# Kernel optimization log

Measured on AMD Instinct MI355X. Metric: run time of the kernel, lower is better.

The kernel has to match this reference:

```python
import jax, jax.numpy as jnp
import numpy as np

B, T, I, H = 64, 2048, 256, 256


def setup_inputs() -> dict:
    key = jax.random.key(0)
    ks = jax.random.split(key, 6)
    s = 1.0 / np.sqrt(H)
    x = jax.random.normal(ks[0], (B, T, I), dtype=jnp.float32)
    att_weights = jax.random.uniform(ks[1], (B, T), dtype=jnp.float32)
    lengths = jax.random.randint(ks[2], (B,), 1, T + 1, dtype=jnp.int32)
    W_ih = jax.random.uniform(ks[3], (3 * H, I), minval=-s, maxval=s, dtype=jnp.float32)
    W_hh = jax.random.uniform(ks[4], (3 * H, H), minval=-s, maxval=s, dtype=jnp.float32)
    b_ih = jax.random.uniform(ks[5], (3 * H,), minval=-s, maxval=s, dtype=jnp.float32)
    b_hh = jax.random.uniform(jax.random.fold_in(key, 7), (3 * H,), minval=-s, maxval=s, dtype=jnp.float32)
    return {"x": x, "att_weights": att_weights, "lengths": lengths,
            "W_ih": W_ih, "W_hh": W_hh, "b_ih": b_ih, "b_hh": b_hh}


def reference(x, att_weights, lengths, W_ih, W_hh, b_ih, b_hh):
    # x: [B, T, I]; att_weights: [B, T]; lengths: [B]
    Bv, Tv, _ = x.shape
    Hv = W_hh.shape[1]
    # Padded equivalent of the packed-sequence loop: update h only while t < length.
    mask = jnp.arange(Tv)[None, :] < lengths[:, None]  # [B, T]

    def step(h, inp):
        xt, wt, mt = inp  # [B, I], [B], [B]
        gi = xt @ W_ih.T + b_ih  # [B, 3H]
        gh = h @ W_hh.T + b_hh   # [B, 3H]
        i_r, i_z, i_n = jnp.split(gi, 3, axis=-1)
        h_r, h_z, h_n = jnp.split(gh, 3, axis=-1)
        r = jax.nn.sigmoid(i_r + h_r)
        z = jax.nn.sigmoid(i_z + h_z)
        n = jnp.tanh(i_n + r * h_n)
        h_new = (1.0 - z) * n + z * h  # GRUCell output
        w = wt[:, None]
        h_gated = w * h_new + (1.0 - w) * h  # attention gating
        h = jnp.where(mt[:, None], h_gated, h)
        return h, None

    h0 = jnp.zeros((Bv, Hv), dtype=x.dtype)
    xs = (jnp.swapaxes(x, 0, 1), att_weights.T, mask.T)  # time-major
    hT, _ = jax.lax.scan(step, h0, xs)
    return hT  # [B, H]
```

## Files before the change

kernel.cpp:

```cpp
#include <hip/hip_runtime.h>
#include <stdint.h>

#define B_ 64
#define T_ 2048
#define I_ 256
#define H_ 256
#define G3 768

typedef _Float16 half2v __attribute__((ext_vector_type(2)));
typedef _Float16 half8v __attribute__((ext_vector_type(8)));

#if __has_builtin(__builtin_amdgcn_fdot2)
#define FDOT2(a, b, c) __builtin_amdgcn_fdot2((a), (b), (c), false)
#else
#define FDOT2(a, b, c) fmaf((float)(a)[1], (float)(b)[1], fmaf((float)(a)[0], (float)(b)[0], (c)))
#endif

__global__ __launch_bounds__(256) void gi_gemm(
    const float* __restrict__ x, const float* __restrict__ Wih,
    const float* __restrict__ bih, const float* __restrict__ bhh,
    float* __restrict__ gi, int t0)
{
  const int t  = t0 + blockIdx.x;
  const int n0 = blockIdx.y * 64;
  __shared__ float As[32][68];
  __shared__ float Bs[32][68];
  const int tid = threadIdx.x;
  const int ty = tid >> 4, tx = tid & 15;
  const int lr = tid >> 3;
  const int lk = (tid & 7) << 2;
  float acc[4][4] = {};

  for (int kc = 0; kc < I_; kc += 32) {
    float4 a0 = *(const float4*)(x + ((size_t)lr        * T_ + t) * I_ + kc + lk);
    float4 a1 = *(const float4*)(x + ((size_t)(lr + 32) * T_ + t) * I_ + kc + lk);
    float4 b0 = *(const float4*)(Wih + (size_t)(n0 + lr)      * I_ + kc + lk);
    float4 b1 = *(const float4*)(Wih + (size_t)(n0 + lr + 32) * I_ + kc + lk);
    __syncthreads();
    As[lk+0][lr]    = a0.x; As[lk+1][lr]    = a0.y; As[lk+2][lr]    = a0.z; As[lk+3][lr]    = a0.w;
    As[lk+0][lr+32] = a1.x; As[lk+1][lr+32] = a1.y; As[lk+2][lr+32] = a1.z; As[lk+3][lr+32] = a1.w;
    Bs[lk+0][lr]    = b0.x; Bs[lk+1][lr]    = b0.y; Bs[lk+2][lr]    = b0.z; Bs[lk+3][lr]    = b0.w;
    Bs[lk+0][lr+32] = b1.x; Bs[lk+1][lr+32] = b1.y; Bs[lk+2][lr+32] = b1.z; Bs[lk+3][lr+32] = b1.w;
    __syncthreads();
    #pragma unroll
    for (int kk = 0; kk < 32; ++kk) {
      float4 av = *(const float4*)(&As[kk][ty << 2]);
      float4 bv = *(const float4*)(&Bs[kk][tx << 2]);
      float av_[4] = {av.x, av.y, av.z, av.w};
      float bv_[4] = {bv.x, bv.y, bv.z, bv.w};
      #pragma unroll
      for (int i = 0; i < 4; ++i)
        #pragma unroll
        for (int u = 0; u < 4; ++u)
          acc[i][u] = fmaf(av_[i], bv_[u], acc[i][u]);
    }
  }

  const int colb = n0 + (tx << 2);
  float4 bi = *(const float4*)(bih + colb);
  float4 bh = *(const float4*)(bhh + colb);
  float4 badd;
  badd.x = bi.x + (colb + 0 < 512 ? bh.x : 0.f);
  badd.y = bi.y + (colb + 1 < 512 ? bh.y : 0.f);
  badd.z = bi.z + (colb + 2 < 512 ? bh.z : 0.f);
  badd.w = bi.w + (colb + 3 < 512 ? bh.w : 0.f);
  float* gout = gi + (size_t)blockIdx.x * 64 * G3;
  #pragma unroll
  for (int i = 0; i < 4; ++i) {
    int bb = (ty << 2) + i;
    float4 o;
    o.x = acc[i][0] + badd.x; o.y = acc[i][1] + badd.y;
    o.z = acc[i][2] + badd.z; o.w = acc[i][3] + badd.w;
    *(float4*)(gout + (size_t)bb * G3 + colb) = o;
  }
}

__global__ __launch_bounds__(512) __attribute__((amdgpu_waves_per_eu(2, 2)))
void gru_seq16(const float* __restrict__ gi, const float* __restrict__ att,
               const int* __restrict__ lengths, const float* __restrict__ Whh,
               const float* __restrict__ bhh, float* __restrict__ hws,
               float* __restrict__ out, int t0, int t1)
{
  const int b   = blockIdx.x;
  const int tid = threadIdx.x;
  const int j   = tid >> 1;
  const int s   = tid & 1;
  const int k0  = s << 7;

  __shared__ _Float16 hbuf[2][272];

  half2v w[192];
  #pragma unroll
  for (int g = 0; g < 3; ++g) {
    const float* row = Whh + (size_t)(g * 256 + j) * H_ + k0;
    #pragma unroll
    for (int q = 0; q < 32; ++q) {
      float4 v = *(const float4*)(row + (q << 2));
      half2v a, c;
      a[0] = (_Float16)v.x; a[1] = (_Float16)v.y;
      c[0] = (_Float16)v.z; c[1] = (_Float16)v.w;
      w[g * 64 + 2 * q]     = a;
      w[g * 64 + 2 * q + 1] = c;
    }
  }

  float bhn = 0.f, h_reg = 0.f;
  if (s == 0) {
    bhn = bhh[512 + j];
    h_reg = (t0 > 0) ? hws[b * H_ + j] : 0.f;
  }
  if (tid < 256) {
    float v = (t0 > 0) ? hws[b * H_ + tid] : 0.f;
    hbuf[0][(tid >> 7) * 136 + (tid & 127)] = (_Float16)v;
  }
  int len = lengths[b]; if (len > t1) len = t1;
  __syncthreads();

  float c_gr = 0.f, c_gz = 0.f, c_gn = 0.f, c_wat = 0.f;
  if (s == 0 && t0 < len) {
    const float* gb = gi + (size_t)b * G3;
    c_gr = gb[j]; c_gz = gb[256 + j]; c_gn = gb[512 + j];
    c_wat = att[(size_t)b * T_ + t0];
  }

  int p = 0;
  for (int t = t0; t < len; ++t) {
    float n_gr = 0.f, n_gz = 0.f, n_gn = 0.f, n_wat = 0.f;
    if (s == 0 && t + 1 < len) {
      const float* gb = gi + ((size_t)(t + 1 - t0) * 64 + b) * G3;
      n_gr = gb[j]; n_gz = gb[256 + j]; n_gn = gb[512 + j];
      n_wat = att[(size_t)b * T_ + t + 1];
    }

    float accr = 0.f, accz = 0.f, accn = 0.f;
    const _Float16* hb = &hbuf[p][s * 136];
    #pragma unroll
    for (int q = 0; q < 16; ++q) {
      half8v hv = *(const half8v*)(hb + (q << 3));
      half2v h0 = __builtin_shufflevector(hv, hv, 0, 1);
      half2v h1 = __builtin_shufflevector(hv, hv, 2, 3);
      half2v h2 = __builtin_shufflevector(hv, hv, 4, 5);
      half2v h3 = __builtin_shufflevector(hv, hv, 6, 7);
      const int qq = q << 2;
      accr = FDOT2(w[qq + 0], h0, accr);
      accr = FDOT2(w[qq + 1], h1, accr);
      accr = FDOT2(w[qq + 2], h2, accr);
      accr = FDOT2(w[qq + 3], h3, accr);
      accz = FDOT2(w[64 + qq + 0], h0, accz);
      accz = FDOT2(w[64 + qq + 1], h1, accz);
      accz = FDOT2(w[64 + qq + 2], h2, accz);
      accz = FDOT2(w[64 + qq + 3], h3, accz);
      accn = FDOT2(w[128 + qq + 0], h0, accn);
      accn = FDOT2(w[128 + qq + 1], h1, accn);
      accn = FDOT2(w[128 + qq + 2], h2, accn);
      accn = FDOT2(w[128 + qq + 3], h3, accn);
    }
    accr += __shfl_xor(accr, 1);
    accz += __shfl_xor(accz, 1);
    accn += __shfl_xor(accn, 1);

    if (s == 0) {
      float r = 1.f / (1.f + __expf(-(accr + c_gr)));
      float z = 1.f / (1.f + __expf(-(accz + c_gz)));
      float e2 = __expf(2.f * (c_gn + r * (accn + bhn)));
      float nn = 1.f - 2.f / (e2 + 1.f);
      float hnew = (1.f - z) * nn + z * h_reg;
      h_reg = c_wat * hnew + (1.f - c_wat) * h_reg;
      hbuf[p ^ 1][(j >> 7) * 136 + (j & 127)] = (_Float16)h_reg;
    }
    __syncthreads();
    p ^= 1;
    c_gr = n_gr; c_gz = n_gz; c_gn = n_gn; c_wat = n_wat;
  }

  if (s == 0) {
    hws[b * H_ + j] = h_reg;
    if (t1 == T_) out[b * H_ + j] = h_reg;
  }
}

extern "C" void kernel_launch(void* const* d_in, const int* in_sizes, int n_in,
                              void* d_out, int out_size, void* d_ws, size_t ws_size,
                              hipStream_t stream)
{
  const float* x       = (const float*)d_in[0];
  const float* att     = (const float*)d_in[1];
  const int*   lengths = (const int*)d_in[2];
  const float* Wih     = (const float*)d_in[3];
  const float* Whh     = (const float*)d_in[4];
  const float* bih     = (const float*)d_in[5];
  const float* bhh     = (const float*)d_in[6];
  float* out = (float*)d_out;

  float* hws = (float*)d_ws;
  float* gi  = (float*)((char*)d_ws + 65536);
  const size_t used0 = 65536;
  const size_t per_t = (size_t)B_ * G3 * sizeof(float);
  size_t avail = ws_size > used0 ? ws_size - used0 : 0;
  int Tc = (int)(avail / per_t);
  if (Tc > T_) Tc = T_;
  if (Tc < 1) Tc = 1;

  for (int t0 = 0; t0 < T_; t0 += Tc) {
    int t1 = t0 + Tc; if (t1 > T_) t1 = T_;
    dim3 g1(t1 - t0, G3 / 64);
    gi_gemm<<<g1, 256, 0, stream>>>(x, Wih, bih, bhh, gi, t0);
    gru_seq16<<<B_, 512, 0, stream>>>(gi, att, lengths, Whh, bhh, hws, out, t0, t1);
  }
}
```

Baseline: 3.418 ms.

## Fuse input GEMM and GRU recurrence into one producer/consumer kernel with flags

Merges the input-projection GEMM and the sequential GRU recurrence into a single launch. 192 producer blocks compute gate pre-activations in 16-timestep chunks and publish per-chunk completion counters. 64 consumer blocks spin-wait on those counters before stepping, and prefetch gate inputs two steps ahead with a 2x unrolled step. The goal is to overlap the GEMM with the serial recurrence instead of running them back to back. This relies on all consumer and producer blocks being co-resident, otherwise the spin-waits can deadlock, and it adds a flag-reset kernel per chunk.

```diff
diff --git a/kernel.cpp b/kernel.cpp
--- a/kernel.cpp
+++ b/kernel.cpp
@@ -6,6 +6,9 @@
 #define I_ 256
 #define H_ 256
 #define G3 768
+#define NPROD 192
+#define CH 16
+#define NTILE_N 6
 
 typedef _Float16 half2v __attribute__((ext_vector_type(2)));
 typedef _Float16 half8v __attribute__((ext_vector_type(8)));
@@ -16,78 +19,93 @@
 #define FDOT2(a, b, c) fmaf((float)(a)[1], (float)(b)[1], fmaf((float)(a)[0], (float)(b)[0], (c)))
 #endif
 
-__global__ __launch_bounds__(256) void gi_gemm(
-    const float* __restrict__ x, const float* __restrict__ Wih,
-    const float* __restrict__ bih, const float* __restrict__ bhh,
-    float* __restrict__ gi, int t0)
+__global__ void zero_flags(int* __restrict__ done, int n)
 {
-  const int t  = t0 + blockIdx.x;
-  const int n0 = blockIdx.y * 64;
-  __shared__ float As[32][68];
-  __shared__ float Bs[32][68];
+  int i = threadIdx.x + blockIdx.x * blockDim.x;
+  if (i < n) __hip_atomic_store(&done[i], 0, __ATOMIC_RELAXED, __HIP_MEMORY_SCOPE_AGENT);
+}
+
+__global__ __launch_bounds__(512) __attribute__((amdgpu_waves_per_eu(2, 2)))
+void fused(const float* __restrict__ x, const float* __restrict__ att,
+           const int* __restrict__ lengths, const float* __restrict__ Wih,
+           const float* __restrict__ Whh, const float* __restrict__ bih,
+           const float* __restrict__ bhh, float* __restrict__ gi,
+           int* __restrict__ done, float* __restrict__ hws,
+           float* __restrict__ out, int t0, int t1)
+{
+  __shared__ __align__(16) float smem[32 * 68 + 32 * 132];
   const int tid = threadIdx.x;
-  const int ty = tid >> 4, tx = tid & 15;
-  const int lr = tid >> 3;
-  const int lk = (tid & 7) << 2;
-  float acc[4][4] = {};
-
-  for (int kc = 0; kc < I_; kc += 32) {
-    float4 a0 = *(const float4*)(x + ((size_t)lr        * T_ + t) * I_ + kc + lk);
-    float4 a1 = *(const float4*)(x + ((size_t)(lr + 32) * T_ + t) * I_ + kc + lk);
-    float4 b0 = *(const float4*)(Wih + (size_t)(n0 + lr)      * I_ + kc + lk);
-    float4 b1 = *(const float4*)(Wih + (size_t)(n0 + lr + 32) * I_ + kc + lk);
-    __syncthreads();
-    As[lk+0][lr]    = a0.x; As[lk+1][lr]    = a0.y; As[lk+2][lr]    = a0.z; As[lk+3][lr]    = a0.w;
-    As[lk+0][lr+32] = a1.x; As[lk+1][lr+32] = a1.y; As[lk+2][lr+32] = a1.z; As[lk+3][lr+32] = a1.w;
-    Bs[lk+0][lr]    = b0.x; Bs[lk+1][lr]    = b0.y; Bs[lk+2][lr]    = b0.z; Bs[lk+3][lr]    = b0.w;
-    Bs[lk+0][lr+32] = b1.x; Bs[lk+1][lr+32] = b1.y; Bs[lk+2][lr+32] = b1.z; Bs[lk+3][lr+32] = b1.w;
-    __syncthreads();
-    #pragma unroll
-    for (int kk = 0; kk < 32; ++kk) {
-      float4 av = *(const float4*)(&As[kk][ty << 2]);
-      float4 bv = *(const float4*)(&Bs[kk][tx << 2]);
-      float av_[4] = {av.x, av.y, av.z, av.w};
-      float bv_[4] = {bv.x, bv.y, bv.z, bv.w};
+  const int Tc = t1 - t0;
+
+  if (blockIdx.x >= B_) {
+    const int pid = blockIdx.x - B_;
+    float* As = smem;
+    float* Bs = smem + 32 * 68;
+    const int ty = tid >> 5, tx = tid & 31;
+    const int lr = tid >> 3;
+    const int lk = (tid & 7) << 2;
+    const int NT = Tc * NTILE_N;
+    for (int i = pid; i < NT; i += NPROD) {
+      const int rel = i / NTILE_N;
+      const int tt  = t0 + rel;
+      const int n0  = (i % NTILE_N) << 7;
+      float acc[4][4] = {};
+      for (int kc = 0; kc < I_; kc += 32) {
+        float4 a0 = *(const float4*)(x + ((size_t)lr * T_ + tt) * I_ + kc + lk);
+        float4 b0 = *(const float4*)(Wih + (size_t)(n0 + lr) * I_ + kc + lk);
+        float4 b1 = *(const float4*)(Wih + (size_t)(n0 + lr + 64) * I_ + kc + lk);
+        __syncthreads();
+        As[(lk + 0) * 68 + lr] = a0.x; As[(lk + 1) * 68 + lr] = a0.y;
+        As[(lk + 2) * 68 + lr] = a0.z; As[(lk + 3) * 68 + lr] = a0.w;
+        Bs[(lk + 0) * 132 + lr] = b0.x; Bs[(lk + 1) * 132 + lr] = b0.y;
+        Bs[(lk + 2) * 132 + lr] = b0.z; Bs[(lk + 3) * 132 + lr] = b0.w;
+        Bs[(lk + 0) * 132 + lr + 64] = b1.x; Bs[(lk + 1) * 132 + lr + 64] = b1.y;
+        Bs[(lk + 2) * 132 + lr + 64] = b1.z; Bs[(lk + 3) * 132 + lr + 64] = b1.w;
+        __syncthreads();
+        #pragma unroll
+        for (int kk = 0; kk < 32; ++kk) {
+          float4 av = *(const float4*)(&As[kk * 68 + (ty << 2)]);
+          float4 bv = *(const float4*)(&Bs[kk * 132 + (tx << 2)]);
+          float av_[4] = {av.x, av.y, av.z, av.w};
+          float bv_[4] = {bv.x, bv.y, bv.z, bv.w};
+          #pragma unroll
+          for (int u = 0; u < 4; ++u)
+            #pragma unroll
+            for (int v = 0; v < 4; ++v)
+              acc[u][v] = fmaf(av_[u], bv_[v], acc[u][v]);
+        }
+      }
+      const int colb = n0 + (tx << 2);
+      float4 bi = *(const float4*)(bih + colb);
+      float4 bh = *(const float4*)(bhh + colb);
+      float4 badd;
+      badd.x = bi.x + (colb + 0 < 512 ? bh.x : 0.f);
+      badd.y = bi.y + (colb + 1 < 512 ? bh.y : 0.f);
+      badd.z = bi.z + (colb + 2 < 512 ? bh.z : 0.f);
+      badd.w = bi.w + (colb + 3 < 512 ? bh.w : 0.f);
+      float* gout = gi + (size_t)rel * B_ * G3;
       #pragma unroll
-      for (int i = 0; i < 4; ++i)
-        #pragma unroll
-        for (int u = 0; u < 4; ++u)
-          acc[i][u] = fmaf(av_[i], bv_[u], acc[i][u]);
+      for (int r = 0; r < 4; ++r) {
+        const int bb = (ty << 2) + r;
+        float4 o;
+        o.x = acc[r][0] + badd.x; o.y = acc[r][1] + badd.y;
+        o.z = acc[r][2] + badd.z; o.w = acc[r][3] + badd.w;
+        *(float4*)(gout + (size_t)bb * G3 + colb) = o;
+      }
+      __syncthreads();
+      if (tid == 0) {
+        __threadfence();
+        __hip_atomic_fetch_add(&done[rel >> 4], 1, __ATOMIC_RELEASE, __HIP_MEMORY_SCOPE_AGENT);
+      }
     }
-  }
-
-  const int colb = n0 + (tx << 2);
-  float4 bi = *(const float4*)(bih + colb);
-  float4 bh = *(const float4*)(bhh + colb);
-  float4 badd;
-  badd.x = bi.x + (colb + 0 < 512 ? bh.x : 0.f);
-  badd.y = bi.y + (colb + 1 < 512 ? bh.y : 0.f);
-  badd.z = bi.z + (colb + 2 < 512 ? bh.z : 0.f);
-  badd.w = bi.w + (colb + 3 < 512 ? bh.w : 0.f);
-  float* gout = gi + (size_t)blockIdx.x * 64 * G3;
-  #pragma unroll
-  for (int i = 0; i < 4; ++i) {
-    int bb = (ty << 2) + i;
-    float4 o;
-    o.x = acc[i][0] + badd.x; o.y = acc[i][1] + badd.y;
-    o.z = acc[i][2] + badd.z; o.w = acc[i][3] + badd.w;
-    *(float4*)(gout + (size_t)bb * G3 + colb) = o;
-  }
-}
-
-__global__ __launch_bounds__(512) __attribute__((amdgpu_waves_per_eu(2, 2)))
-void gru_seq16(const float* __restrict__ gi, const float* __restrict__ att,
-               const int* __restrict__ lengths, const float* __restrict__ Whh,
-               const float* __restrict__ bhh, float* __restrict__ hws,
-               float* __restrict__ out, int t0, int t1)
-{
-  const int b   = blockIdx.x;
-  const int tid = threadIdx.x;
-  const int j   = tid >> 1;
-  const int s   = tid & 1;
-  const int k0  = s << 7;
-
-  __shared__ _Float16 hbuf[2][272];
+    return;
+  }
+
+  const int b  = blockIdx.x;
+  const int j  = tid >> 1;
+  const int s  = tid & 1;
+  const int k0 = s << 7;
+  _Float16* hbuf = (_Float16*)smem;
 
   half2v w[192];
   #pragma unroll
@@ -111,72 +129,106 @@
   }
   if (tid < 256) {
     float v = (t0 > 0) ? hws[b * H_ + tid] : 0.f;
-    hbuf[0][(tid >> 7) * 136 + (tid & 127)] = (_Float16)v;
+    hbuf[(tid >> 7) * 136 + (tid & 127)] = (_Float16)v;
   }
   int len = lengths[b]; if (len > t1) len = t1;
+  const int nch = (Tc + CH - 1) / CH;
+  int wm = -1;
   __syncthreads();
 
-  float c_gr = 0.f, c_gz = 0.f, c_gn = 0.f, c_wat = 0.f;
+#define GATE(NEED) do {                                                               \
+    int need_ = (NEED); if (need_ > nch - 1) need_ = nch - 1;                         \
+    if (need_ > wm) {                                                                 \
+      if (tid == 0) {                                                                 \
+        for (int c_ = wm + 1; c_ <= need_; ++c_) {                                    \
+          int exp_ = ((Tc - c_ * CH) < CH ? (Tc - c_ * CH) : CH) * NTILE_N;           \
+          while (__hip_atomic_load(&done[c_], __ATOMIC_RELAXED,                       \
+                                   __HIP_MEMORY_SCOPE_AGENT) < exp_)                  \
+            __builtin_amdgcn_s_sleep(2);                                              \
+        }                                                                             \
+      }                                                                               \
+      __syncthreads();                                                                \
+      __threadfence();             \
+      wm = need_;                                                                     \
+    }                                                                                 \
+  } while (0)
+
+#define STEP(GR, GZ, GN, WAT, TT, RELOAD_OK) do {                                     \
+    float accr = 0.f, accz = 0.f, accn = 0.f;                                         \
+    const _Float16* hb = hbuf + p * 272 + s * 136;                                    \
+    _Pragma("unroll")                                                                 \
+    for (int q = 0; q < 16; ++q) {                                                    \
+      half8v hv = *(const half8v*)(hb + (q << 3));                                    \
+      half2v h0_ = __builtin_shufflevector(hv, hv, 0, 1);                             \
+      half2v h1_ = __builtin_shufflevector(hv, hv, 2, 3);                             \
+      half2v h2_ = __builtin_shufflevector(hv, hv, 4, 5);                             \
+      half2v h3_ = __builtin_shufflevector(hv, hv, 6, 7);                             \
+      const int qq = q << 2;                                                          \
+      accr = FDOT2(w[qq + 0], h0_, accr);                                             \
+      accr = FDOT2(w[qq + 1], h1_, accr);                                             \
+      accr = FDOT2(w[qq + 2], h2_, accr);                                             \
+      accr = FDOT2(w[qq + 3], h3_, accr);                                             \
+      accz = FDOT2(w[64 + qq + 0], h0_, accz);                                        \
+      accz = FDOT2(w[64 + qq + 1], h1_, accz);                                        \
+      accz = FDOT2(w[64 + qq + 2], h2_, accz);                                        \
+      accz = FDOT2(w[64 + qq + 3], h3_, accz);                                        \
+      accn = FDOT2(w[128 + qq + 0], h0_, accn);                                       \
+      accn = FDOT2(w[128 + qq + 1], h1_, accn);                                       \
+      accn = FDOT2(w[128 + qq + 2], h2_, accn);                                       \
+      accn = FDOT2(w[128 + qq + 3], h3_, accn);                                       \
+    }                                                                                 \
+    accr += __shfl_xor(accr, 1);                                                      \
+    accz += __shfl_xor(accz, 1);                                                      \
+    accn += __shfl_xor(accn, 1);                                                      \
+    if (s == 0) {                                                                     \
+      float r_ = 1.f / (1.f + __expf(-(accr + GR)));                                  \
+      float z_ = 1.f / (1.f + __expf(-(accz + GZ)));                                  \
+      float e2_ = __expf(2.f * (GN + r_ * (accn + bhn)));                             \
+      float nn_ = 1.f - 2.f / (e2_ + 1.f);                                            \
+      float hnew_ = (1.f - z_) * nn_ + z_ * h_reg;                                    \
+      h_reg = (WAT) * hnew_ + (1.f - (WAT)) * h_reg;                                  \
+      hbuf[(p ^ 1) * 272 + (j >> 7) * 136 + (j & 127)] = (_Float16)h_reg;             \
+      if (RELOAD_OK) {                                                                \
+        const float* gb_ = gi + ((size_t)((TT) + 2 - t0) * B_ + b) * G3;              \
+        GR = gb_[j]; GZ = gb_[256 + j]; GN = gb_[512 + j];                            \
+        WAT = att[(size_t)b * T_ + (TT) + 2];                                         \
+      }                                                                               \
+    }                                                                                 \
+    __syncthreads();                                                                  \
+    p ^= 1;                                                                           \
+  } while (0)
+
+  GATE(0);
+  float e_gr = 0.f, e_gz = 0.f, e_gn = 0.f, e_wat = 0.f;
+  float o_gr = 0.f, o_gz = 0.f, o_gn = 0.f, o_wat = 0.f;
   if (s == 0 && t0 < len) {
     const float* gb = gi + (size_t)b * G3;
-    c_gr = gb[j]; c_gz = gb[256 + j]; c_gn = gb[512 + j];
-    c_wat = att[(size_t)b * T_ + t0];
+    e_gr = gb[j]; e_gz = gb[256 + j]; e_gn = gb[512 + j];
+    e_wat = att[(size_t)b * T_ + t0];
+  }
+  if (s == 0 && t0 + 1 < len) {
+    const float* gb = gi + ((size_t)B_ + b) * G3;
+    o_gr = gb[j]; o_gz = gb[256 + j]; o_gn = gb[512 + j];
+    o_wat = att[(size_t)b * T_ + t0 + 1];
   }
 
   int p = 0;
-  for (int t = t0; t < len; ++t) {
-    float n_gr = 0.f, n_gz = 0.f, n_gn = 0.f, n_wat = 0.f;
-    if (s == 0 && t + 1 < len) {
-      const float* gb = gi + ((size_t)(t + 1 - t0) * 64 + b) * G3;
-      n_gr = gb[j]; n_gz = gb[256 + j]; n_gn = gb[512 + j];
-      n_wat = att[(size_t)b * T_ + t + 1];
-    }
-
-    float accr = 0.f, accz = 0.f, accn = 0.f;
-    const _Float16* hb = &hbuf[p][s * 136];
-    #pragma unroll
-    for (int q = 0; q < 16; ++q) {
-      half8v hv = *(const half8v*)(hb + (q << 3));
-      half2v h0 = __builtin_shufflevector(hv, hv, 0, 1);
-      half2v h1 = __builtin_shufflevector(hv, hv, 2, 3);
-      half2v h2 = __builtin_shufflevector(hv, hv, 4, 5);
-      half2v h3 = __builtin_shufflevector(hv, hv, 6, 7);
-      const int qq = q << 2;
-      accr = FDOT2(w[qq + 0], h0, accr);
-      accr = FDOT2(w[qq + 1], h1, accr);
-      accr = FDOT2(w[qq + 2], h2, accr);
-      accr = FDOT2(w[qq + 3], h3, accr);
-      accz = FDOT2(w[64 + qq + 0], h0, accz);
-      accz = FDOT2(w[64 + qq + 1], h1, accz);
-      accz = FDOT2(w[64 + qq + 2], h2, accz);
-      accz = FDOT2(w[64 + qq + 3], h3, accz);
-      accn = FDOT2(w[128 + qq + 0], h0, accn);
-      accn = FDOT2(w[128 + qq + 1], h1, accn);
-      accn = FDOT2(w[128 + qq + 2], h2, accn);
-      accn = FDOT2(w[128 + qq + 3], h3, accn);
-    }
-    accr += __shfl_xor(accr, 1);
-    accz += __shfl_xor(accz, 1);
-    accn += __shfl_xor(accn, 1);
-
-    if (s == 0) {
-      float r = 1.f / (1.f + __expf(-(accr + c_gr)));
-      float z = 1.f / (1.f + __expf(-(accz + c_gz)));
-      float e2 = __expf(2.f * (c_gn + r * (accn + bhn)));
-      float nn = 1.f - 2.f / (e2 + 1.f);
-      float hnew = (1.f - z) * nn + z * h_reg;
-      h_reg = c_wat * hnew + (1.f - c_wat) * h_reg;
-      hbuf[p ^ 1][(j >> 7) * 136 + (j & 127)] = (_Float16)h_reg;
-    }
-    __syncthreads();
-    p ^= 1;
-    c_gr = n_gr; c_gz = n_gz; c_gn = n_gn; c_wat = n_wat;
+  int t = t0;
+  for (; t + 1 < len; t += 2) {
+    GATE((t + 3 - t0) >> 4);
+    STEP(e_gr, e_gz, e_gn, e_wat, t,     (t + 2 < len));
+    STEP(o_gr, o_gz, o_gn, o_wat, t + 1, (t + 3 < len));
+  }
+  if (t < len) {
+    STEP(e_gr, e_gz, e_gn, e_wat, t, false);
   }
 
   if (s == 0) {
     hws[b * H_ + j] = h_reg;
     if (t1 == T_) out[b * H_ + j] = h_reg;
   }
+#undef STEP
+#undef GATE
 }
 
 extern "C" void kernel_launch(void* const* d_in, const int* in_sizes, int n_in,
@@ -192,9 +244,10 @@
   const float* bhh     = (const float*)d_in[6];
   float* out = (float*)d_out;
 
-  float* hws = (float*)d_ws;
-  float* gi  = (float*)((char*)d_ws + 65536);
-  const size_t used0 = 65536;
+  int*   done = (int*)d_ws;
+  float* hws  = (float*)((char*)d_ws + 4096);
+  float* gi   = (float*)((char*)d_ws + 4096 + 65536);
+  const size_t used0 = 4096 + 65536;
   const size_t per_t = (size_t)B_ * G3 * sizeof(float);
   size_t avail = ws_size > used0 ? ws_size - used0 : 0;
   int Tc = (int)(avail / per_t);
@@ -203,8 +256,9 @@
 
   for (int t0 = 0; t0 < T_; t0 += Tc) {
     int t1 = t0 + Tc; if (t1 > T_) t1 = T_;
-    dim3 g1(t1 - t0, G3 / 64);
-    gi_gemm<<<g1, 256, 0, stream>>>(x, Wih, bih, bhh, gi, t0);
-    gru_seq16<<<B_, 512, 0, stream>>>(gi, att, lengths, Whh, bhh, hws, out, t0, t1);
+    int nch = (t1 - t0 + CH - 1) / CH;
+    zero_flags<<<dim3((nch + 127) / 128), 128, 0, stream>>>(done, nch);
+    fused<<<dim3(B_ + NPROD), 512, 0, stream>>>(x, att, lengths, Wih, Whh, bih, bhh,
+                                                gi, done, hws, out, t0, t1);
   }
 }
```

Result: slower. 3.738 ms (+9.3%).
